# Kernel optimization log

Measured on AMD Instinct MI355X. Metric: run time of the kernel, lower is better.

The kernel has to match this reference:

```python
import jax, jax.numpy as jnp
import numpy as np

G = 16          # horizontal stripes
K = 4           # latents per stripe
TEMP = 0.125
TOPK_RATIO = 0.125
GATE_THR = 0.05
EPS = 1e-6
KSZ = 3


def setup_inputs() -> dict:
    key = jax.random.key(0)
    k1, k2 = jax.random.split(key)
    x = jax.random.normal(k1, (64, 256, 64, 44), dtype=jnp.float32)
    latent_basis = jax.random.normal(k2, (G, K, 256), dtype=jnp.float32)
    return {"x": x, "latent_basis": latent_basis}


def _avg_pool3(x):
    # x: [n, g, c, sh, w]; 3x3 avg pool, stride 1, pad 1, count_include_pad=True
    s = jax.lax.reduce_window(x, 0.0, jax.lax.add,
                              (1, 1, 1, KSZ, KSZ), (1, 1, 1, 1, 1),
                              [(0, 0), (0, 0), (0, 0), (1, 1), (1, 1)])
    return s / float(KSZ * KSZ)


def _l2norm(v, axis=-1):
    return v / jnp.maximum(jnp.linalg.norm(v, axis=axis, keepdims=True), 1e-12)


def reference(x, latent_basis):
    n, c, h, w = x.shape
    sh = h // G
    p = sh * w
    # split into horizontal stripes: [n, g, c, sh, w]
    xr = x.reshape(n, c, G, sh, w).transpose(0, 2, 1, 3, 4)
    support_feat = _avg_pool3(xr)
    feat_flat = xr.transpose(0, 1, 3, 4, 2).reshape(n, G, p, c)          # ngpc
    support_flat = support_feat.transpose(0, 1, 3, 4, 2).reshape(n, G, p, c)

    # active mask from detached feature energy
    e = jax.lax.stop_gradient(xr).astype(jnp.float32)
    fe = jnp.mean(e * e, axis=2)                                          # n g sh w
    fe = fe / jnp.maximum(jnp.max(fe, axis=(-2, -1), keepdims=True), EPS)
    active = (fe > GATE_THR).astype(jnp.float32)
    fallback = (fe > 0).astype(jnp.float32)
    use_fb = jnp.sum(active, axis=(-2, -1), keepdims=True) <= 0
    active = jnp.where(use_fb, fallback, active).reshape(n, G, p)

    # cosine-similarity routing
    sfn = _l2norm(support_flat)
    lbn = _l2norm(latent_basis)                                           # g k c
    logits = jnp.einsum('ngpc,gkc->ngpk', sfn, lbn) / TEMP
    route_prob = jax.nn.softmax(logits, axis=-1)
    support = route_prob * active[..., None]                              # n g p k
    pool_w = support / jnp.maximum(jnp.sum(support, axis=2, keepdims=True), EPS)
    tokens = jnp.einsum('ngpk,ngpc->ngkc', pool_w, feat_flat)
    tokens = tokens.transpose(0, 3, 1, 2).reshape(n, c, G * K)            # n c (g k)

    # top-k presence
    kk = max(1, min(p, int(p * TOPK_RATIO)))
    topv, _ = jax.lax.top_k(support.transpose(0, 1, 3, 2), kk)            # n g k kk
    presence = jnp.mean(topv, axis=-1).reshape(n, G * K)
    presence = presence / jnp.maximum(jnp.sum(presence, axis=1, keepdims=True), EPS)

    # scatter per-stripe maps back into full-resolution zero tensors
    eye = jnp.eye(G, dtype=support.dtype)
    loc_s = support.reshape(n, G, sh, w, K).transpose(0, 1, 4, 2, 3)      # n g k sh w
    loc_p = pool_w.reshape(n, G, sh, w, K).transpose(0, 1, 4, 2, 3)
    smap = jnp.einsum('ngksw,gG->ngkGsw', loc_s, eye).reshape(n, G * K, h, w)
    pmap = jnp.einsum('ngksw,gG->ngkGsw', loc_p, eye).reshape(n, G * K, h, w)
    support_flat_global = smap.transpose(0, 2, 3, 1).reshape(n, h * w, G * K)
    pool_weights_flat_global = pmap.transpose(0, 2, 3, 1).reshape(n, h * w, G * K)

    return (tokens.astype(x.dtype), presence.astype(x.dtype),
            support_flat_global.astype(x.dtype), pool_weights_flat_global.astype(x.dtype))
```

## Files before the change

kernel.cpp:

```cpp
#include <hip/hip_runtime.h>
#include <math.h>

#define GG   16
#define KK   4
#define NN   64
#define CC   256
#define SHH  4
#define WW   44
#define PP   176
#define HWSZ 2816
#define CHW  720896
#define TOPKK 22

template<int CTRL, int RMASK>
__device__ __forceinline__ float dpp0(float v) {
    return __int_as_float(__builtin_amdgcn_update_dpp(
        0, __float_as_int(v), CTRL, RMASK, 0xF, true));
}
__device__ __forceinline__ float nbrL(float v) { return dpp0<0x138, 0xF>(v); }
__device__ __forceinline__ float nbrR(float v) { return dpp0<0x130, 0xF>(v); }

__device__ __forceinline__ float wave_sum63(float v) {
    v += dpp0<0x111, 0xF>(v);
    v += dpp0<0x112, 0xF>(v);
    v += dpp0<0x114, 0xF>(v);
    v += dpp0<0x118, 0xF>(v);
    v += dpp0<0x142, 0xA>(v);
    v += dpp0<0x143, 0xC>(v);
    return v;
}
__device__ __forceinline__ float bcast63(float v) {
    return __int_as_float(__builtin_amdgcn_readlane(__float_as_int(v), 63));
}
__device__ __forceinline__ float wave_sum_all(float v) { return bcast63(wave_sum63(v)); }

__device__ __forceinline__ float wave_max_nn(float v) {
    v = fmaxf(v, dpp0<0x111, 0xF>(v));
    v = fmaxf(v, dpp0<0x112, 0xF>(v));
    v = fmaxf(v, dpp0<0x114, 0xF>(v));
    v = fmaxf(v, dpp0<0x118, 0xF>(v));
    v = fmaxf(v, dpp0<0x142, 0xA>(v));
    v = fmaxf(v, dpp0<0x143, 0xC>(v));
    return bcast63(v);
}

__global__ __launch_bounds__(64) void norm_basis_kernel(
    const float* __restrict__ lb, float* __restrict__ lbn) {
    const int gk = blockIdx.x;
    const int lane = threadIdx.x;
    const float* row = lb + (size_t)gk * CC;
    float v0 = row[lane], v1 = row[lane + 64], v2 = row[lane + 128], v3 = row[lane + 192];
    float ss = v0 * v0 + v1 * v1 + v2 * v2 + v3 * v3;
    float tot = wave_sum_all(ss);
    float sc = 1.0f / fmaxf(sqrtf(tot), 1e-12f);
    const int g = gk >> 2, k = gk & 3;
    float* dst = lbn + (size_t)g * CC * 4 + k;
    dst[(size_t)lane * 4]         = v0 * sc;
    dst[(size_t)(lane + 64) * 4]  = v1 * sc;
    dst[(size_t)(lane + 128) * 4] = v2 * sc;
    dst[(size_t)(lane + 192) * 4] = v3 * sc;
}

__global__ __launch_bounds__(512, 8) void fused_kernel(
    const float* __restrict__ x, const float* __restrict__ lbn,
    float* __restrict__ pres_ws, float* __restrict__ tok_out,
    float4* __restrict__ outS, float4* __restrict__ outP) {
    const int g = blockIdx.x;
    const int n = blockIdx.y;
    const int tid = threadIdx.x;
    const int w = tid >> 6;
    const int lane = tid & 63;
    const bool al = lane < WW;

    __shared__ float4 pd[8][PP];
    __shared__ float2 pnf[8][PP];
    __shared__ float redA[4], redB[4], zred[4][4];
    float4* sup4 = pd[2];
    float4* pw4  = pd[4];

    const float* xb = x + (size_t)n * CHW + g * PP;
    const float4* lbg = (const float4*)lbn + (g << 8);

    float4 dk[4];
    float nr[4] = {0, 0, 0, 0}, fe[4] = {0, 0, 0, 0};
    #pragma unroll
    for (int s = 0; s < 4; ++s) dk[s] = make_float4(0, 0, 0, 0);

    const int c0 = w * 32;
    float r0 = 0, r1 = 0, r2 = 0, r3 = 0;
    if (al) {
        const float* xc = xb + (size_t)c0 * HWSZ;
        r0 = xc[lane]; r1 = xc[lane + 44]; r2 = xc[lane + 88]; r3 = xc[lane + 132];
    }
    #pragma unroll 1
    for (int i = 0; i < 32; ++i) {
        float b0 = 0, b1 = 0, b2 = 0, b3 = 0;
        if (i < 31 && al) {
            const float* xn = xb + (size_t)(c0 + i + 1) * HWSZ;
            b0 = xn[lane]; b1 = xn[lane + 44]; b2 = xn[lane + 88]; b3 = xn[lane + 132];
        }
        float4 lb = lbg[c0 + i];
        fe[0] += r0 * r0; fe[1] += r1 * r1; fe[2] += r2 * r2; fe[3] += r3 * r3;
        float h0 = r0 + nbrL(r0) + nbrR(r0);
        float h1 = r1 + nbrL(r1) + nbrR(r1);
        float h2 = r2 + nbrL(r2) + nbrR(r2);
        float h3 = r3 + nbrL(r3) + nbrR(r3);
        const float k9 = 1.0f / 9.0f;
        float p0 = (h0 + h1) * k9;
        float p1 = (h0 + h1 + h2) * k9;
        float p2 = (h1 + h2 + h3) * k9;
        float p3 = (h2 + h3) * k9;
        nr[0] += p0 * p0; nr[1] += p1 * p1; nr[2] += p2 * p2; nr[3] += p3 * p3;
        dk[0].x += p0 * lb.x; dk[0].y += p0 * lb.y; dk[0].z += p0 * lb.z; dk[0].w += p0 * lb.w;
        dk[1].x += p1 * lb.x; dk[1].y += p1 * lb.y; dk[1].z += p1 * lb.z; dk[1].w += p1 * lb.w;
        dk[2].x += p2 * lb.x; dk[2].y += p2 * lb.y; dk[2].z += p2 * lb.z; dk[2].w += p2 * lb.w;
        dk[3].x += p3 * lb.x; dk[3].y += p3 * lb.y; dk[3].z += p3 * lb.z; dk[3].w += p3 * lb.w;
        r0 = b0; r1 = b1; r2 = b2; r3 = b3;
    }
    if (al) {
        #pragma unroll
        for (int s = 0; s < 4; ++s) {
            pd[w][s * 44 + lane]  = dk[s];
            pnf[w][s * 44 + lane] = make_float2(nr[s], fe[s]);
        }
    }
    __syncthreads();

    if (tid < PP) {
        float4 a = pd[0][tid];
        #pragma unroll
        for (int ww = 1; ww < 8; ++ww) {
            float4 b = pd[ww][tid];
            a.x += b.x; a.y += b.y; a.z += b.z; a.w += b.w;
        }
        pd[0][tid] = a;
    } else if (tid >= 256 && tid < 256 + PP) {
        const int p = tid - 256;
        float2 a = pnf[0][p];
        #pragma unroll
        for (int ww = 1; ww < 8; ++ww) {
            float2 b = pnf[ww][p];
            a.x += b.x; a.y += b.y;
        }
        pnf[0][p] = a;
    }
    __syncthreads();

    const int s4 = w & 3;
    const int pix = s4 * 44 + (al ? lane : 0);
    float4 dv = pd[0][pix];
    float2 nf = pnf[0][pix];
    float nrm = nf.x;
    float fev = nf.y * (1.0f / 256.0f);

    float fmw = wave_max_nn(al ? fev : 0.0f);
    if (w < 4 && lane == 0) redA[s4] = fmw;
    __syncthreads();
    float femax = fmaxf(fmaxf(redA[0], redA[1]), fmaxf(redA[2], redA[3]));
    float den = fmaxf(femax, 1e-6f);
    bool pa = al && ((fev / den) > 0.05f);
    unsigned long long bl = __ballot((int)pa);
    if (w < 4 && lane == 0) redB[s4] = (float)__popcll(bl);
    __syncthreads();
    float cnt = redB[0] + redB[1] + redB[2] + redB[3];
    float actv = pa ? 1.0f : 0.0f;
    if (cnt <= 0.0f) actv = (al && (fev > 0.0f)) ? 1.0f : 0.0f;

    float inv = 8.0f / fmaxf(sqrtf(nrm), 1e-12f);
    float L0 = dv.x * inv, L1 = dv.y * inv, L2 = dv.z * inv, L3 = dv.w * inv;
    float mx = fmaxf(fmaxf(L0, L1), fmaxf(L2, L3));
    float e0 = expf(L0 - mx), e1 = expf(L1 - mx), e2 = expf(L2 - mx), e3 = expf(L3 - mx);
    float esum = e0 + e1 + e2 + e3;
    float sc = actv / esum;
    float s0 = e0 * sc, s1 = e1 * sc, s2 = e2 * sc, s3 = e3 * sc;

    float z0 = wave_sum63(s0), z1 = wave_sum63(s1), z2 = wave_sum63(s2), z3 = wave_sum63(s3);
    if (w < 4 && lane == 63) { zred[s4][0] = z0; zred[s4][1] = z1; zred[s4][2] = z2; zred[s4][3] = z3; }
    __syncthreads();
    float Z0 = zred[0][0] + zred[1][0] + zred[2][0] + zred[3][0];
    float Z1 = zred[0][1] + zred[1][1] + zred[2][1] + zred[3][1];
    float Z2 = zred[0][2] + zred[1][2] + zred[2][2] + zred[3][2];
    float Z3 = zred[0][3] + zred[1][3] + zred[2][3] + zred[3][3];
    float q0 = s0 / fmaxf(Z0, 1e-6f);
    float q1 = s1 / fmaxf(Z1, 1e-6f);
    float q2 = s2 / fmaxf(Z2, 1e-6f);
    float q3 = s3 / fmaxf(Z3, 1e-6f);

    if (w < 4 && al) {
        sup4[pix] = make_float4(s0, s1, s2, s3);
        pw4[pix]  = make_float4(q0, q1, q2, q3);
    }
    __syncthreads();

    if (w < 4) {
        const float* supf = (const float*)sup4;
        const int k = w;
        float v0 = supf[lane * 4 + k];
        float v1 = supf[(lane + 64) * 4 + k];
        float v2 = (lane < PP - 128) ? supf[(lane + 128) * 4 + k] : -1e30f;
        float tks = 0.0f;
        for (int it = 0; it < TOPKK; ++it) {
            float lm = fmaxf(v0, fmaxf(v1, v2));
            float M = wave_max_nn(lm);
            tks += M;
            unsigned long long mk = __ballot((int)(lm == M));
            int src = __ffsll(mk) - 1;
            if (lane == src) {
                if (v0 == M)      v0 = -1e30f;
                else if (v1 == M) v1 = -1e30f;
                else              v2 = -1e30f;
            }
        }
        if (lane == 0) pres_ws[(size_t)n * 64 + g * KK + k] = tks * (1.0f / (float)TOPKK);
    }

    {
        const size_t obase = ((size_t)n * HWSZ + (size_t)g * PP) * 16;
        const float4 z = make_float4(0, 0, 0, 0);
        #pragma unroll 1
        for (int j = tid; j < PP * 16; j += 512) {
            const int px = j >> 4, q = j & 15;
            float4 vs = sup4[px];
            float4 vp = pw4[px];
            bool hit = (q == g);
            outS[obase + j] = hit ? vs : z;
            outP[obase + j] = hit ? vp : z;
        }
    }

    {
        float4 pwa = pw4[lane];
        float4 pwb = pw4[lane + 64];
        float4 pwc = (lane < PP - 128) ? pw4[lane + 128] : make_float4(0, 0, 0, 0);
        float* tokg = tok_out + (size_t)n * CC * 64 + g * KK;
        const int cb = w * 32;
        const float* xc0 = xb + (size_t)cb * HWSZ;
        float a0 = xc0[lane];
        float a1 = xc0[lane + 64];
        float a2 = (lane < PP - 128) ? xc0[lane + 128] : 0.0f;
        #pragma unroll 1
        for (int i = 0; i < 32; ++i) {
            float b0 = 0, b1 = 0, b2 = 0;
            if (i < 31) {
                const float* xn = xb + (size_t)(cb + i + 1) * HWSZ;
                b0 = xn[lane]; b1 = xn[lane + 64];
                b2 = (lane < PP - 128) ? xn[lane + 128] : 0.0f;
            }
            float t0 = a0 * pwa.x + a1 * pwb.x + a2 * pwc.x;
            float t1 = a0 * pwa.y + a1 * pwb.y + a2 * pwc.y;
            float t2 = a0 * pwa.z + a1 * pwb.z + a2 * pwc.z;
            float t3 = a0 * pwa.w + a1 * pwb.w + a2 * pwc.w;
            t0 = wave_sum63(t0); t1 = wave_sum63(t1); t2 = wave_sum63(t2); t3 = wave_sum63(t3);
            if (lane == 63) {
                *(float4*)(tokg + (size_t)(cb + i) * 64) = make_float4(t0, t1, t2, t3);
            }
            a0 = b0; a1 = b1; a2 = b2;
        }
    }
}

__global__ __launch_bounds__(64) void presence_kernel(
    const float* __restrict__ pres_ws, float* __restrict__ outp) {
    const int n = blockIdx.x;
    const int lane = threadIdx.x;
    float v = pres_ws[(size_t)n * 64 + lane];
    float tot = wave_sum_all(v);
    outp[(size_t)n * 64 + lane] = v / fmaxf(tot, 1e-6f);
}

extern "C" void kernel_launch(void* const* d_in, const int* in_sizes, int n_in,
                              void* d_out, int out_size, void* d_ws, size_t ws_size,
                              hipStream_t stream) {
    const float* x = (const float*)d_in[0];
    const float* lb = (const float*)d_in[1];
    float* ws = (float*)d_ws;
    float* lbn     = ws;
    float* pres_ws = lbn + 16384;

    float* out = (float*)d_out;
    float* tok  = out;
    float* pres = out + 1048576;
    float* outS = out + 1052672;
    float* outP = outS + 11534336;

    norm_basis_kernel<<<GG * KK, 64, 0, stream>>>(lb, lbn);
    fused_kernel<<<dim3(GG, NN), 512, 0, stream>>>(
        x, lbn, pres_ws, tok, (float4*)outS, (float4*)outP);
    presence_kernel<<<NN, 64, 0, stream>>>(pres_ws, pres);
}
```

Measured before the change: 358.4 us.

## Split fused kernel into routing, token, and scatter kernels for more parallelism

Breaks the monolithic per-(n,g) kernel into three launches. The routing kernel writes support and pool weights to workspace, a token kernel spreads the channel reduction over four times as many blocks, and a separate scatter kernel writes the large zero-padded output maps. The 1/9 pooling scale is folded into the normalized basis and the logit scale, and warp index and pointer arithmetic are simplified. The aim is to raise occupancy and parallelism for the token reduction and the output writes. In exchange x is read from memory twice and the support and pool weights make an extra round trip through workspace.

```diff
diff --git a/kernel.cpp b/kernel.cpp
--- a/kernel.cpp
+++ b/kernel.cpp
@@ -52,7 +52,7 @@
     float v0 = row[lane], v1 = row[lane + 64], v2 = row[lane + 128], v3 = row[lane + 192];
     float ss = v0 * v0 + v1 * v1 + v2 * v2 + v3 * v3;
     float tot = wave_sum_all(ss);
-    float sc = 1.0f / fmaxf(sqrtf(tot), 1e-12f);
+    float sc = (1.0f / 9.0f) / fmaxf(sqrtf(tot), 1e-12f);
     const int g = gk >> 2, k = gk & 3;
     float* dst = lbn + (size_t)g * CC * 4 + k;
     dst[(size_t)lane * 4]         = v0 * sc;
@@ -61,14 +61,14 @@
     dst[(size_t)(lane + 192) * 4] = v3 * sc;
 }
 
-__global__ __launch_bounds__(512, 8) void fused_kernel(
+__global__ __launch_bounds__(512, 8) void routing_kernel(
     const float* __restrict__ x, const float* __restrict__ lbn,
-    float* __restrict__ pres_ws, float* __restrict__ tok_out,
-    float4* __restrict__ outS, float4* __restrict__ outP) {
+    float* __restrict__ sup_ws, float* __restrict__ pw_ws,
+    float* __restrict__ pres_ws) {
     const int g = blockIdx.x;
     const int n = blockIdx.y;
     const int tid = threadIdx.x;
-    const int w = tid >> 6;
+    const int w = __builtin_amdgcn_readfirstlane(tid >> 6);
     const int lane = tid & 63;
     const bool al = lane < WW;
 
@@ -79,42 +79,39 @@
     float4* pw4  = pd[4];
 
     const float* xb = x + (size_t)n * CHW + g * PP;
-    const float4* lbg = (const float4*)lbn + (g << 8);
+    const int c0 = w * 32;
+    const float4* lbq = (const float4*)lbn + (g << 8) + c0;
 
     float4 dk[4];
     float nr[4] = {0, 0, 0, 0}, fe[4] = {0, 0, 0, 0};
     #pragma unroll
     for (int s = 0; s < 4; ++s) dk[s] = make_float4(0, 0, 0, 0);
 
-    const int c0 = w * 32;
+    const float* xp = xb + (size_t)c0 * HWSZ + lane;
     float r0 = 0, r1 = 0, r2 = 0, r3 = 0;
-    if (al) {
-        const float* xc = xb + (size_t)c0 * HWSZ;
-        r0 = xc[lane]; r1 = xc[lane + 44]; r2 = xc[lane + 88]; r3 = xc[lane + 132];
-    }
+    if (al) { r0 = xp[0]; r1 = xp[44]; r2 = xp[88]; r3 = xp[132]; }
+    xp += HWSZ;
     #pragma unroll 1
     for (int i = 0; i < 32; ++i) {
         float b0 = 0, b1 = 0, b2 = 0, b3 = 0;
-        if (i < 31 && al) {
-            const float* xn = xb + (size_t)(c0 + i + 1) * HWSZ;
-            b0 = xn[lane]; b1 = xn[lane + 44]; b2 = xn[lane + 88]; b3 = xn[lane + 132];
-        }
-        float4 lb = lbg[c0 + i];
+        if (i < 31 && al) { b0 = xp[0]; b1 = xp[44]; b2 = xp[88]; b3 = xp[132]; }
+        xp += HWSZ;
+        float4 lbv = lbq[i];
         fe[0] += r0 * r0; fe[1] += r1 * r1; fe[2] += r2 * r2; fe[3] += r3 * r3;
         float h0 = r0 + nbrL(r0) + nbrR(r0);
         float h1 = r1 + nbrL(r1) + nbrR(r1);
         float h2 = r2 + nbrL(r2) + nbrR(r2);
         float h3 = r3 + nbrL(r3) + nbrR(r3);
-        const float k9 = 1.0f / 9.0f;
-        float p0 = (h0 + h1) * k9;
-        float p1 = (h0 + h1 + h2) * k9;
-        float p2 = (h1 + h2 + h3) * k9;
-        float p3 = (h2 + h3) * k9;
+        float p0 = h0 + h1;
+        float p1 = p0 + h2;
+        float t23 = h2 + h3;
+        float p2 = h1 + t23;
+        float p3 = t23;
         nr[0] += p0 * p0; nr[1] += p1 * p1; nr[2] += p2 * p2; nr[3] += p3 * p3;
-        dk[0].x += p0 * lb.x; dk[0].y += p0 * lb.y; dk[0].z += p0 * lb.z; dk[0].w += p0 * lb.w;
-        dk[1].x += p1 * lb.x; dk[1].y += p1 * lb.y; dk[1].z += p1 * lb.z; dk[1].w += p1 * lb.w;
-        dk[2].x += p2 * lb.x; dk[2].y += p2 * lb.y; dk[2].z += p2 * lb.z; dk[2].w += p2 * lb.w;
-        dk[3].x += p3 * lb.x; dk[3].y += p3 * lb.y; dk[3].z += p3 * lb.z; dk[3].w += p3 * lb.w;
+        dk[0].x += p0 * lbv.x; dk[0].y += p0 * lbv.y; dk[0].z += p0 * lbv.z; dk[0].w += p0 * lbv.w;
+        dk[1].x += p1 * lbv.x; dk[1].y += p1 * lbv.y; dk[1].z += p1 * lbv.z; dk[1].w += p1 * lbv.w;
+        dk[2].x += p2 * lbv.x; dk[2].y += p2 * lbv.y; dk[2].z += p2 * lbv.z; dk[2].w += p2 * lbv.w;
+        dk[3].x += p3 * lbv.x; dk[3].y += p3 * lbv.y; dk[3].z += p3 * lbv.z; dk[3].w += p3 * lbv.w;
         r0 = b0; r1 = b1; r2 = b2; r3 = b3;
     }
     if (al) {
@@ -166,7 +163,7 @@
     float actv = pa ? 1.0f : 0.0f;
     if (cnt <= 0.0f) actv = (al && (fev > 0.0f)) ? 1.0f : 0.0f;
 
-    float inv = 8.0f / fmaxf(sqrtf(nrm), 1e-12f);
+    float inv = 72.0f / fmaxf(sqrtf(nrm), 9e-12f);
     float L0 = dv.x * inv, L1 = dv.y * inv, L2 = dv.z * inv, L3 = dv.w * inv;
     float mx = fmaxf(fmaxf(L0, L1), fmaxf(L2, L3));
     float e0 = expf(L0 - mx), e1 = expf(L1 - mx), e2 = expf(L2 - mx), e3 = expf(L3 - mx);
@@ -187,8 +184,13 @@
     float q3 = s3 / fmaxf(Z3, 1e-6f);
 
     if (w < 4 && al) {
-        sup4[pix] = make_float4(s0, s1, s2, s3);
-        pw4[pix]  = make_float4(q0, q1, q2, q3);
+        float4 sv = make_float4(s0, s1, s2, s3);
+        float4 qv = make_float4(q0, q1, q2, q3);
+        sup4[pix] = sv;
+        pw4[pix]  = qv;
+        const size_t wsb = (size_t)(n * GG + g) * PP + pix;
+        ((float4*)sup_ws)[wsb] = sv;
+        ((float4*)pw_ws)[wsb]  = qv;
     }
     __syncthreads();
 
@@ -213,49 +215,68 @@
         }
         if (lane == 0) pres_ws[(size_t)n * 64 + g * KK + k] = tks * (1.0f / (float)TOPKK);
     }
-
-    {
-        const size_t obase = ((size_t)n * HWSZ + (size_t)g * PP) * 16;
-        const float4 z = make_float4(0, 0, 0, 0);
-        #pragma unroll 1
-        for (int j = tid; j < PP * 16; j += 512) {
-            const int px = j >> 4, q = j & 15;
-            float4 vs = sup4[px];
-            float4 vp = pw4[px];
-            bool hit = (q == g);
-            outS[obase + j] = hit ? vs : z;
-            outP[obase + j] = hit ? vp : z;
-        }
-    }
-
-    {
-        float4 pwa = pw4[lane];
-        float4 pwb = pw4[lane + 64];
-        float4 pwc = (lane < PP - 128) ? pw4[lane + 128] : make_float4(0, 0, 0, 0);
-        float* tokg = tok_out + (size_t)n * CC * 64 + g * KK;
-        const int cb = w * 32;
-        const float* xc0 = xb + (size_t)cb * HWSZ;
-        float a0 = xc0[lane];
-        float a1 = xc0[lane + 64];
-        float a2 = (lane < PP - 128) ? xc0[lane + 128] : 0.0f;
-        #pragma unroll 1
-        for (int i = 0; i < 32; ++i) {
-            float b0 = 0, b1 = 0, b2 = 0;
-            if (i < 31) {
-                const float* xn = xb + (size_t)(cb + i + 1) * HWSZ;
-                b0 = xn[lane]; b1 = xn[lane + 64];
-                b2 = (lane < PP - 128) ? xn[lane + 128] : 0.0f;
-            }
-            float t0 = a0 * pwa.x + a1 * pwb.x + a2 * pwc.x;
-            float t1 = a0 * pwa.y + a1 * pwb.y + a2 * pwc.y;
-            float t2 = a0 * pwa.z + a1 * pwb.z + a2 * pwc.z;
-            float t3 = a0 * pwa.w + a1 * pwb.w + a2 * pwc.w;
-            t0 = wave_sum63(t0); t1 = wave_sum63(t1); t2 = wave_sum63(t2); t3 = wave_sum63(t3);
-            if (lane == 63) {
-                *(float4*)(tokg + (size_t)(cb + i) * 64) = make_float4(t0, t1, t2, t3);
-            }
-            a0 = b0; a1 = b1; a2 = b2;
-        }
+}
+
+__global__ __launch_bounds__(256, 8) void token_kernel(
+    const float* __restrict__ x, const float* __restrict__ pw_ws,
+    float* __restrict__ tok_out) {
+    const int g = blockIdx.x & 15;
+    const int chunk = blockIdx.x >> 4;
+    const int n = blockIdx.y;
+    const int w = __builtin_amdgcn_readfirstlane(threadIdx.x >> 6);
+    const int lane = threadIdx.x & 63;
+
+    const float4* pwq = (const float4*)pw_ws + (size_t)(n * GG + g) * PP;
+    float4 pwa = pwq[lane];
+    float4 pwb = pwq[lane + 64];
+    float4 pwc = (lane < 48) ? pwq[lane + 128] : make_float4(0, 0, 0, 0);
+
+    const int cb = chunk * 64 + w * 16;
+    const float* xp = x + (size_t)n * CHW + g * PP + (size_t)cb * HWSZ + lane;
+    float* tokg = tok_out + (size_t)n * CC * 64 + g * KK + (size_t)cb * 64;
+
+    float a0 = xp[0];
+    float a1 = xp[64];
+    float a2 = (lane < 48) ? xp[128] : 0.0f;
+    xp += HWSZ;
+    #pragma unroll 1
+    for (int i = 0; i < 16; ++i) {
+        float b0 = 0, b1 = 0, b2 = 0;
+        if (i < 15) {
+            b0 = xp[0]; b1 = xp[64];
+            if (lane < 48) b2 = xp[128];
+        }
+        xp += HWSZ;
+        float t0 = a0 * pwa.x + a1 * pwb.x + a2 * pwc.x;
+        float t1 = a0 * pwa.y + a1 * pwb.y + a2 * pwc.y;
+        float t2 = a0 * pwa.z + a1 * pwb.z + a2 * pwc.z;
+        float t3 = a0 * pwa.w + a1 * pwb.w + a2 * pwc.w;
+        t0 = wave_sum63(t0); t1 = wave_sum63(t1); t2 = wave_sum63(t2); t3 = wave_sum63(t3);
+        if (lane == 63) {
+            *(float4*)(tokg + (size_t)i * 64) = make_float4(t0, t1, t2, t3);
+        }
+        a0 = b0; a1 = b1; a2 = b2;
+    }
+}
+
+__global__ __launch_bounds__(256, 8) void scatter_kernel(
+    const float4* __restrict__ sup_ws4, const float4* __restrict__ pw_ws4,
+    float4* __restrict__ outS, float4* __restrict__ outP) {
+    const int g = blockIdx.x;
+    const int n = blockIdx.y;
+    const int t = threadIdx.x;
+    __shared__ float4 ls[PP], lp[PP];
+    const size_t wsb = (size_t)(n * GG + g) * PP;
+    if (t < PP) { ls[t] = sup_ws4[wsb + t]; lp[t] = pw_ws4[wsb + t]; }
+    __syncthreads();
+    const size_t obase = ((size_t)n * HWSZ + (size_t)g * PP) * 16;
+    const float4 z = make_float4(0, 0, 0, 0);
+    #pragma unroll 1
+    for (int j = t; j < PP * 16; j += 256) {
+        const int px = j >> 4, q = j & 15;
+        const bool hit = (q == g);
+        outS[obase + j] = hit ? ls[px] : z;
+        outP[obase + j] = hit ? lp[px] : z;
     }
 }
 
@@ -276,6 +297,8 @@
     float* ws = (float*)d_ws;
     float* lbn     = ws;
     float* pres_ws = lbn + 16384;
+    float* sup_ws  = pres_ws + 4096;
+    float* pw_ws   = sup_ws + 720896;
 
     float* out = (float*)d_out;
     float* tok  = out;
@@ -284,7 +307,9 @@
     float* outP = outS + 11534336;
 
     norm_basis_kernel<<<GG * KK, 64, 0, stream>>>(lb, lbn);
-    fused_kernel<<<dim3(GG, NN), 512, 0, stream>>>(
-        x, lbn, pres_ws, tok, (float4*)outS, (float4*)outP);
+    routing_kernel<<<dim3(GG, NN), 512, 0, stream>>>(x, lbn, sup_ws, pw_ws, pres_ws);
+    token_kernel<<<dim3(GG * 4, NN), 256, 0, stream>>>(x, pw_ws, tok);
+    scatter_kernel<<<dim3(GG, NN), 256, 0, stream>>>(
+        (const float4*)sup_ws, (const float4*)pw_ws, (float4*)outS, (float4*)outP);
     presence_kernel<<<NN, 64, 0, stream>>>(pres_ws, pres);
 }
```

Measured after the change: 342.6 us. -4.4%, faster.
